# Kernel tuning notes

Hardware: AMD Instinct MI355X
Metric: run time of the kernel (lower is better)

The kernel has to match this reference:

```python
import jax, jax.numpy as jnp
import numpy as np

K = 5      # kernel_size
STRIDE = 1
EPS = 1e-7


def _extract_patches(x, k, s):
    # x: [B,H,W,C] -> [B,Ho,Wo,k,k,C], same (kh,kw,c) layout as tf.extract_image_patches VALID
    B, H, W, C = x.shape
    Ho = (H - k) // s + 1
    Wo = (W - k) // s + 1
    r = (jnp.arange(Ho) * s)[:, None] + jnp.arange(k)   # [Ho,k]
    c = (jnp.arange(Wo) * s)[:, None] + jnp.arange(k)   # [Wo,k]
    return x[:, r[:, None, :, None], c[None, :, None, :], :]


def _rotate(pflat, angle, k):
    # Replicates tf.contrib.image.transform with angles_to_projective_transforms,
    # including the (1+1e-7) normalization of the 3x3 matrix in the original code.
    # pflat: [N, k*k, C], angle: [N]; bilinear sampling, fill value 0 outside.
    N = pflat.shape[0]
    f32 = pflat.dtype
    co, si = jnp.cos(angle), jnp.sin(angle)
    km1 = jnp.asarray(k - 1, f32)
    xoff = (km1 - (co * km1 - si * km1)) * 0.5
    yoff = (km1 - (si * km1 + co * km1)) * 0.5
    scale = 1.0 / (1.0 + EPS)  # transforms /= transforms[:, 8:9] + 1e-7
    gy, gx = jnp.meshgrid(jnp.arange(k, dtype=f32), jnp.arange(k, dtype=f32), indexing='ij')
    sx = (co[:, None, None] * gx - si[:, None, None] * gy + xoff[:, None, None]) * scale
    sy = (si[:, None, None] * gx + co[:, None, None] * gy + yoff[:, None, None]) * scale
    sx = sx.reshape(N, k * k)
    sy = sy.reshape(N, k * k)
    x0 = jnp.floor(sx)
    y0 = jnp.floor(sy)
    wx = (sx - x0)[..., None]
    wy = (sy - y0)[..., None]
    x0i = x0.astype(jnp.int32)
    y0i = y0.astype(jnp.int32)

    def samp(yi, xi):
        valid = (xi >= 0) & (xi < k) & (yi >= 0) & (yi < k)
        idx = jnp.clip(yi, 0, k - 1) * k + jnp.clip(xi, 0, k - 1)   # [N,k*k]
        v = jnp.take_along_axis(pflat, idx[..., None], axis=1)      # [N,k*k,C]
        return jnp.where(valid[..., None], v, jnp.zeros((), f32))

    v00 = samp(y0i, x0i)
    v01 = samp(y0i, x0i + 1)
    v10 = samp(y0i + 1, x0i)
    v11 = samp(y0i + 1, x0i + 1)
    top = v00 * (1 - wx) + v01 * wx
    bot = v10 * (1 - wx) + v11 * wx
    return top * (1 - wy) + bot * wy   # [N,k*k,C]


def _forward(input_tensor, W, b):
    k, s = K, STRIDE
    B, H, Wd, C = input_tensor.shape
    patches = _extract_patches(input_tensor, k, s)      # [B,Ho,Wo,k,k,C]
    Ho, Wo = patches.shape[1], patches.shape[2]
    inten = patches.sum(-1)                             # [B,Ho,Wo,k,k] channel-sum intensity
    ridx = jnp.arange(k, dtype=patches.dtype)
    tot = inten.sum((-2, -1)) + EPS
    cr = (inten * ridx[:, None]).sum((-2, -1)) / tot    # centroid row
    cc = (inten * ridx[None, :]).sum((-2, -1)) / tot    # centroid col
    m = (k - 1) / 2.0                                   # meanCenter (same for row/col)
    angle = jnp.arctan2(cr - m, cc - m + EPS)           # [B,Ho,Wo]
    pflat = patches.reshape(B * Ho * Wo, k * k, C)
    rot = _rotate(pflat, angle.reshape(-1), k)          # [N,k*k,C]
    rot = rot.reshape(B, Ho * Wo, k * k * C)
    wflat = W.reshape(W.shape[0], -1)                   # [F, k*k*C]
    out = jnp.einsum('bpd,fd->bpf', rot, wflat)         # elementwise-mult-sum 'conv'
    return out.reshape(B, Ho, Wo, -1) + b


def setup_inputs():
    key = jax.random.key(0)
    k1, k2 = jax.random.split(key, 2)
    B, H, Wd, C, F = 4, 128, 128, 16, 32
    input_tensor = jax.random.uniform(k1, (B, H, Wd, C), dtype=jnp.float32)
    lim = float(np.sqrt(6.0 / (K * K * C + F)))  # glorot_uniform
    W = jax.random.uniform(k2, (F, K, K, C), minval=-lim, maxval=lim, dtype=jnp.float32)
    b = jnp.zeros((F,), jnp.float32)
    return {"input_tensor": input_tensor, "W": W, "b": b}


def reference(input_tensor, W, b):
    return _forward(input_tensor, W, b)
```

## Files before the change

kernel.cpp:

```cpp
#include <hip/hip_runtime.h>


#define KS     5
#define TILE   8
#define NPIX   64
#define TW     (TILE + KS - 1)
#define CPAD   20
#define C_IN   16
#define F_OUT  32
#define H_IN   128
#define W_IN   128
#define HO     124
#define WO     124
#define NBATCH 4
#define EPSF   1e-7f
#define BLOCK  256
#define NCHUNK 7
#define AROW   72
#define KW     400

typedef __attribute__((ext_vector_type(8))) short  short8;
typedef __attribute__((ext_vector_type(4))) float  floatx4;

static __device__ __forceinline__ short f2bf(float f) {
    union { float f; unsigned u; } v; v.f = f;
    unsigned r = v.u + 0x7fffu + ((v.u >> 16) & 1u);
    return (short)(r >> 16);
}

__global__ __launch_bounds__(BLOCK) void rotconv_kernel(
    const float* __restrict__ in, const float* __restrict__ Wg,
    const float* __restrict__ bg, float* __restrict__ out)
{
    __shared__ float s_in[TW * TW * CPAD];
    __shared__ float s_int[TW * (TW + 1)];
    __shared__ short sA[NPIX * AROW];

    const int tid  = threadIdx.x;
    const int bx = blockIdx.x, by = blockIdx.y, bimg = blockIdx.z;
    const int ox = bx * TILE, oy = by * TILE;

    const float* inb = in + (size_t)bimg * (H_IN * W_IN * C_IN);
    for (int i = tid; i < TW * TW * (C_IN / 4); i += BLOCK) {
        int cv = i & 3;
        int pp = i >> 2;
        int x = pp % TW, y = pp / TW;
        int gy = oy + y, gx = ox + x;
        float4 v = make_float4(0.f, 0.f, 0.f, 0.f);
        if (gy < H_IN && gx < W_IN)
            v = *(const float4*)(inb + ((size_t)(gy * W_IN + gx) * C_IN) + 4 * cv);
        *(float4*)(&s_in[pp * CPAD + 4 * cv]) = v;
    }
    __syncthreads();

    for (int pp = tid; pp < TW * TW; pp += BLOCK) {
        const float* sp = &s_in[pp * CPAD];
        float s = 0.f;
        #pragma unroll
        for (int c = 0; c < C_IN; ++c) s += sp[c];
        s_int[(pp / TW) * (TW + 1) + (pp % TW)] = s;
    }
    __syncthreads();

    const int p    = tid & 63;
    const int wv   = tid >> 6;
    const int lx   = p & 7, ly = p >> 3;
    const int col  = p & 15;
    const int quad = p >> 4;

    float tot = EPSF, cr = 0.f, cc = 0.f;
    #pragma unroll
    for (int dy = 0; dy < KS; ++dy)
        #pragma unroll
        for (int dx = 0; dx < KS; ++dx) {
            float v = s_int[(ly + dy) * (TW + 1) + (lx + dx)];
            tot += v; cr += v * (float)dy; cc += v * (float)dx;
        }
    cr /= tot; cc /= tot;
    float ang = atan2f(cr - 2.0f, cc - 2.0f + EPSF);
    float si, co;
    sincosf(ang, &si, &co);
    const float scl = 1.0f / (1.0f + EPSF);
    float xoff = (4.0f - (co * 4.0f - si * 4.0f)) * 0.5f;
    float yoff = (4.0f - (si * 4.0f + co * 4.0f)) * 0.5f;

    const int nt  = wv >> 1;
    const int mt0 = (wv & 1) * 2;

    floatx4 acc0, acc1;
    {
        float bv = bg[nt * 16 + col];
        acc0 = (floatx4){bv, bv, bv, bv};
        acc1 = acc0;
    }

    for (int ch = 0; ch < NCHUNK; ++ch) {
        int t = 4 * ch + wv;
        short8 alo = {0,0,0,0,0,0,0,0}, ahi = {0,0,0,0,0,0,0,0};
        if (t < KS * KS) {
            int ky = t / KS, kx = t - KS * ky;
            float sx = (co * (float)kx - si * (float)ky + xoff) * scl;
            float sy = (si * (float)kx + co * (float)ky + yoff) * scl;
            float fx0 = floorf(sx), fy0 = floorf(sy);
            float wx = sx - fx0, wy = sy - fy0;
            int x0 = (int)fx0, y0 = (int)fy0;
            int x1 = x0 + 1, y1 = y0 + 1;
            float vx0 = (x0 >= 0 && x0 < KS) ? 1.f : 0.f;
            float vx1 = (x1 >= 0 && x1 < KS) ? 1.f : 0.f;
            float vy0 = (y0 >= 0 && y0 < KS) ? 1.f : 0.f;
            float vy1 = (y1 >= 0 && y1 < KS) ? 1.f : 0.f;
            float w00 = (1.f - wx) * (1.f - wy) * vx0 * vy0;
            float w01 = wx * (1.f - wy) * vx1 * vy0;
            float w10 = (1.f - wx) * wy * vx0 * vy1;
            float w11 = wx * wy * vx1 * vy1;
            int cx0 = min(max(x0, 0), KS - 1), cx1 = min(max(x1, 0), KS - 1);
            int cy0 = min(max(y0, 0), KS - 1), cy1 = min(max(y1, 0), KS - 1);
            const float* p00 = &s_in[((ly + cy0) * TW + (lx + cx0)) * CPAD];
            const float* p01 = &s_in[((ly + cy0) * TW + (lx + cx1)) * CPAD];
            const float* p10 = &s_in[((ly + cy1) * TW + (lx + cx0)) * CPAD];
            const float* p11 = &s_in[((ly + cy1) * TW + (lx + cx1)) * CPAD];
            float r[16];
            #pragma unroll
            for (int cv = 0; cv < 4; ++cv) {
                float4 a = *(const float4*)(p00 + 4 * cv);
                float4 b = *(const float4*)(p01 + 4 * cv);
                float4 c = *(const float4*)(p10 + 4 * cv);
                float4 d = *(const float4*)(p11 + 4 * cv);
                r[4*cv+0] = w00 * a.x + w01 * b.x + w10 * c.x + w11 * d.x;
                r[4*cv+1] = w00 * a.y + w01 * b.y + w10 * c.y + w11 * d.y;
                r[4*cv+2] = w00 * a.z + w01 * b.z + w10 * c.z + w11 * d.z;
                r[4*cv+3] = w00 * a.w + w01 * b.w + w10 * c.w + w11 * d.w;
            }
            alo = (short8){f2bf(r[0]), f2bf(r[1]), f2bf(r[2]), f2bf(r[3]),
                           f2bf(r[4]), f2bf(r[5]), f2bf(r[6]), f2bf(r[7])};
            ahi = (short8){f2bf(r[8]),  f2bf(r[9]),  f2bf(r[10]), f2bf(r[11]),
                           f2bf(r[12]), f2bf(r[13]), f2bf(r[14]), f2bf(r[15])};
        }
        __syncthreads();
        *(short8*)(&sA[p * AROW + wv * 16])     = alo;
        *(short8*)(&sA[p * AROW + wv * 16 + 8]) = ahi;
        __syncthreads();

        int nk = (ch == NCHUNK - 1) ? 1 : 2;
        for (int kk = 0; kk < nk; ++kk) {
            int kg = ch * 64 + kk * 32 + quad * 8;
            short8 bf = {0,0,0,0,0,0,0,0};
            if (kg + 8 <= KW) {
                const float* wp = Wg + (size_t)(nt * 16 + col) * KW + kg;
                float4 a = *(const float4*)(wp);
                float4 b = *(const float4*)(wp + 4);
                bf = (short8){f2bf(a.x), f2bf(a.y), f2bf(a.z), f2bf(a.w),
                              f2bf(b.x), f2bf(b.y), f2bf(b.z), f2bf(b.w)};
            }
            short8 a0 = *(const short8*)(&sA[(16 * mt0 + col) * AROW + kk * 32 + quad * 8]);
            short8 a1 = *(const short8*)(&sA[(16 * mt0 + 16 + col) * AROW + kk * 32 + quad * 8]);
            acc0 = __builtin_amdgcn_mfma_f32_16x16x32_bf16(a0, bf, acc0, 0, 0, 0);
            acc1 = __builtin_amdgcn_mfma_f32_16x16x32_bf16(a1, bf, acc1, 0, 0, 0);
        }
    }

    #pragma unroll
    for (int r = 0; r < 4; ++r) {
        int pix0 = 16 * mt0 + quad * 4 + r;
        int ho = oy + (pix0 >> 3), wo = ox + (pix0 & 7);
        if (ho < HO && wo < WO)
            out[(((size_t)bimg * HO + ho) * WO + wo) * F_OUT + nt * 16 + col] = acc0[r];
        int pix1 = pix0 + 16;
        ho = oy + (pix1 >> 3); wo = ox + (pix1 & 7);
        if (ho < HO && wo < WO)
            out[(((size_t)bimg * HO + ho) * WO + wo) * F_OUT + nt * 16 + col] = acc1[r];
    }
}

extern "C" void kernel_launch(void* const* d_in, const int* in_sizes, int n_in,
                              void* d_out, int out_size, void* d_ws, size_t ws_size,
                              hipStream_t stream) {
    const float* in = (const float*)d_in[0];
    const float* Wg = (const float*)d_in[1];
    const float* bg = (const float*)d_in[2];
    float* out      = (float*)d_out;
    dim3 grid((WO + TILE - 1) / TILE, (HO + TILE - 1) / TILE, NBATCH);
    rotconv_kernel<<<grid, dim3(BLOCK), 0, stream>>>(in, Wg, bg, out);
}
```

Before: 76.15 us.

## Preload bf16 weight fragments into registers and double-buffer the A tile

Weight fragments for all K steps are loaded and converted to bf16 once at kernel start and kept in registers, rather than reloaded from global memory every chunk. The shared A tile is double-buffered, which removes one of the two barriers per chunk. The chunk loop is fully unrolled and launch bounds request 4 blocks per SM. The 13 short8 fragments add register pressure that could cut occupancy or cause spills.

```diff
diff --git a/kernel.cpp b/kernel.cpp
--- a/kernel.cpp
+++ b/kernel.cpp
@@ -16,6 +16,7 @@
 #define EPSF   1e-7f
 #define BLOCK  256
 #define NCHUNK 7
+#define NKSTEP 13
 #define AROW   72
 #define KW     400
 
@@ -28,17 +29,42 @@
     return (short)(r >> 16);
 }
 
-__global__ __launch_bounds__(BLOCK) void rotconv_kernel(
+__global__ __launch_bounds__(BLOCK, 4) void rotconv_kernel(
     const float* __restrict__ in, const float* __restrict__ Wg,
     const float* __restrict__ bg, float* __restrict__ out)
 {
     __shared__ float s_in[TW * TW * CPAD];
     __shared__ float s_int[TW * (TW + 1)];
-    __shared__ short sA[NPIX * AROW];
+    __shared__ short sA[2][NPIX * AROW];
 
     const int tid  = threadIdx.x;
     const int bx = blockIdx.x, by = blockIdx.y, bimg = blockIdx.z;
     const int ox = bx * TILE, oy = by * TILE;
+
+    const int p    = tid & 63;
+    const int wv   = tid >> 6;
+    const int lx   = p & 7, ly = p >> 3;
+    const int col  = p & 15;
+    const int quad = p >> 4;
+    const int nt   = wv >> 1;
+    const int mt0  = (wv & 1) * 2;
+
+    short8 wfrag[NKSTEP];
+    {
+        const float* wrow = Wg + (size_t)(nt * 16 + col) * KW;
+        #pragma unroll
+        for (int s = 0; s < NKSTEP; ++s) {
+            int kg = s * 32 + quad * 8;
+            short8 bf = {0,0,0,0,0,0,0,0};
+            if (kg + 8 <= KW) {
+                float4 a = *(const float4*)(wrow + kg);
+                float4 b = *(const float4*)(wrow + kg + 4);
+                bf = (short8){f2bf(a.x), f2bf(a.y), f2bf(a.z), f2bf(a.w),
+                              f2bf(b.x), f2bf(b.y), f2bf(b.z), f2bf(b.w)};
+            }
+            wfrag[s] = bf;
+        }
+    }
 
     const float* inb = in + (size_t)bimg * (H_IN * W_IN * C_IN);
     for (int i = tid; i < TW * TW * (C_IN / 4); i += BLOCK) {
@@ -62,12 +88,6 @@
     }
     __syncthreads();
 
-    const int p    = tid & 63;
-    const int wv   = tid >> 6;
-    const int lx   = p & 7, ly = p >> 3;
-    const int col  = p & 15;
-    const int quad = p >> 4;
-
     float tot = EPSF, cr = 0.f, cc = 0.f;
     #pragma unroll
     for (int dy = 0; dy < KS; ++dy)
@@ -84,9 +104,6 @@
     float xoff = (4.0f - (co * 4.0f - si * 4.0f)) * 0.5f;
     float yoff = (4.0f - (si * 4.0f + co * 4.0f)) * 0.5f;
 
-    const int nt  = wv >> 1;
-    const int mt0 = (wv & 1) * 2;
-
     floatx4 acc0, acc1;
     {
         float bv = bg[nt * 16 + col];
@@ -94,6 +111,7 @@
         acc1 = acc0;
     }
 
+    #pragma unroll
     for (int ch = 0; ch < NCHUNK; ++ch) {
         int t = 4 * ch + wv;
         short8 alo = {0,0,0,0,0,0,0,0}, ahi = {0,0,0,0,0,0,0,0};
@@ -136,26 +154,20 @@
             ahi = (short8){f2bf(r[8]),  f2bf(r[9]),  f2bf(r[10]), f2bf(r[11]),
                            f2bf(r[12]), f2bf(r[13]), f2bf(r[14]), f2bf(r[15])};
         }
-        __syncthreads();
-        *(short8*)(&sA[p * AROW + wv * 16])     = alo;
-        *(short8*)(&sA[p * AROW + wv * 16 + 8]) = ahi;
+        short* buf = &sA[ch & 1][0];
+        *(short8*)(&buf[p * AROW + wv * 16])     = alo;
+        *(short8*)(&buf[p * AROW + wv * 16 + 8]) = ahi;
         __syncthreads();
 
-        int nk = (ch == NCHUNK - 1) ? 1 : 2;
-        for (int kk = 0; kk < nk; ++kk) {
-            int kg = ch * 64 + kk * 32 + quad * 8;
-            short8 bf = {0,0,0,0,0,0,0,0};
-            if (kg + 8 <= KW) {
-                const float* wp = Wg + (size_t)(nt * 16 + col) * KW + kg;
-                float4 a = *(const float4*)(wp);
-                float4 b = *(const float4*)(wp + 4);
-                bf = (short8){f2bf(a.x), f2bf(a.y), f2bf(a.z), f2bf(a.w),
-                              f2bf(b.x), f2bf(b.y), f2bf(b.z), f2bf(b.w)};
+        #pragma unroll
+        for (int kk = 0; kk < 2; ++kk) {
+            int s = ch * 2 + kk;
+            if (s < NKSTEP) {
+                short8 a0 = *(const short8*)(&buf[(16 * mt0 + col) * AROW + kk * 32 + quad * 8]);
+                short8 a1 = *(const short8*)(&buf[(16 * mt0 + 16 + col) * AROW + kk * 32 + quad * 8]);
+                acc0 = __builtin_amdgcn_mfma_f32_16x16x32_bf16(a0, wfrag[s], acc0, 0, 0, 0);
+                acc1 = __builtin_amdgcn_mfma_f32_16x16x32_bf16(a1, wfrag[s], acc1, 0, 0, 0);
             }
-            short8 a0 = *(const short8*)(&sA[(16 * mt0 + col) * AROW + kk * 32 + quad * 8]);
-            short8 a1 = *(const short8*)(&sA[(16 * mt0 + 16 + col) * AROW + kk * 32 + quad * 8]);
-            acc0 = __builtin_amdgcn_mfma_f32_16x16x32_bf16(a0, bf, acc0, 0, 0, 0);
-            acc1 = __builtin_amdgcn_mfma_f32_16x16x32_bf16(a1, bf, acc1, 0, 0, 0);
         }
     }
 
```

After: 90.36 us. 1.19x slower.

## Split-K across waves with 32x32 MFMA and shared bf16 weights

Applied to the files above, without the earlier changes.

Each wave now keeps the samples it computes for its own filter taps in registers and runs 32x32x16 bf16 MFMAs over all 64 pixels and 32 filters. This removes the per-chunk LDS staging of the A operand and the two barriers per chunk. The bf16-converted weights are preloaded once per block into shared memory, and the four partial accumulators are reduced through LDS at the end, with wave 0 adding the bias and writing the output. The trade-offs are larger accumulators (32 VGPRs per wave), a final LDS reduction, a cross-lane shuffle to assemble the A fragments, and a launch-bounds occupancy hint.

```diff
diff --git a/kernel.cpp b/kernel.cpp
--- a/kernel.cpp
+++ b/kernel.cpp
@@ -3,7 +3,6 @@
 
 #define KS     5
 #define TILE   8
-#define NPIX   64
 #define TW     (TILE + KS - 1)
 #define CPAD   20
 #define C_IN   16
@@ -15,30 +14,48 @@
 #define NBATCH 4
 #define EPSF   1e-7f
 #define BLOCK  256
-#define NCHUNK 7
-#define AROW   72
+#define NTAP   25
 #define KW     400
 
-typedef __attribute__((ext_vector_type(8))) short  short8;
-typedef __attribute__((ext_vector_type(4))) float  floatx4;
+typedef __attribute__((ext_vector_type(8)))  short short8;
+typedef __attribute__((ext_vector_type(16))) float floatx16;
 
-static __device__ __forceinline__ short f2bf(float f) {
+static __device__ __forceinline__ unsigned f2bfu(float f) {
     union { float f; unsigned u; } v; v.f = f;
     unsigned r = v.u + 0x7fffu + ((v.u >> 16) & 1u);
-    return (short)(r >> 16);
+    return r >> 16;
+}
+static __device__ __forceinline__ unsigned pack2(float a, float b) {
+    return f2bfu(a) | (f2bfu(b) << 16);
 }
 
-__global__ __launch_bounds__(BLOCK) void rotconv_kernel(
+__global__ __launch_bounds__(BLOCK, 4) void rotconv_kernel(
     const float* __restrict__ in, const float* __restrict__ Wg,
     const float* __restrict__ bg, float* __restrict__ out)
 {
     __shared__ float s_in[TW * TW * CPAD];
     __shared__ float s_int[TW * (TW + 1)];
-    __shared__ short sA[NPIX * AROW];
+    __shared__ union {
+        short w[NTAP * 64 * 8];
+        float red[3 * 2048];
+    } uW;
 
     const int tid  = threadIdx.x;
     const int bx = blockIdx.x, by = blockIdx.y, bimg = blockIdx.z;
     const int ox = bx * TILE, oy = by * TILE;
+    const int p  = tid & 63;
+    const int wv = __builtin_amdgcn_readfirstlane(tid >> 6);
+    const int lx = p & 7, ly = p >> 3;
+
+    for (int i = tid; i < NTAP * 64; i += BLOCK) {
+        int t = i >> 6, l = i & 63;
+        const float* wp = Wg + (size_t)(l & 31) * KW + t * 16 + (l >> 5) * 8;
+        float4 a = *(const float4*)(wp);
+        float4 b = *(const float4*)(wp + 4);
+        unsigned* d = (unsigned*)&uW.w[i * 8];
+        d[0] = pack2(a.x, a.y); d[1] = pack2(a.z, a.w);
+        d[2] = pack2(b.x, b.y); d[3] = pack2(b.z, b.w);
+    }
 
     const float* inb = in + (size_t)bimg * (H_IN * W_IN * C_IN);
     for (int i = tid; i < TW * TW * (C_IN / 4); i += BLOCK) {
@@ -62,12 +79,6 @@
     }
     __syncthreads();
 
-    const int p    = tid & 63;
-    const int wv   = tid >> 6;
-    const int lx   = p & 7, ly = p >> 3;
-    const int col  = p & 15;
-    const int quad = p >> 4;
-
     float tot = EPSF, cr = 0.f, cc = 0.f;
     #pragma unroll
     for (int dy = 0; dy < KS; ++dy)
@@ -84,20 +95,11 @@
     float xoff = (4.0f - (co * 4.0f - si * 4.0f)) * 0.5f;
     float yoff = (4.0f - (si * 4.0f + co * 4.0f)) * 0.5f;
 
-    const int nt  = wv >> 1;
-    const int mt0 = (wv & 1) * 2;
+    floatx16 acc0 = {0}, acc1 = {0};
 
-    floatx4 acc0, acc1;
-    {
-        float bv = bg[nt * 16 + col];
-        acc0 = (floatx4){bv, bv, bv, bv};
-        acc1 = acc0;
-    }
-
-    for (int ch = 0; ch < NCHUNK; ++ch) {
-        int t = 4 * ch + wv;
-        short8 alo = {0,0,0,0,0,0,0,0}, ahi = {0,0,0,0,0,0,0,0};
-        if (t < KS * KS) {
+    for (int i = 0; i < 7; ++i) {
+        int t = wv + 4 * i;
+        if (t < NTAP) {
             int ky = t / KS, kx = t - KS * ky;
             float sx = (co * (float)kx - si * (float)ky + xoff) * scl;
             float sy = (si * (float)kx + co * (float)ky + yoff) * scl;
@@ -131,44 +133,54 @@
                 r[4*cv+2] = w00 * a.z + w01 * b.z + w10 * c.z + w11 * d.z;
                 r[4*cv+3] = w00 * a.w + w01 * b.w + w10 * c.w + w11 * d.w;
             }
-            alo = (short8){f2bf(r[0]), f2bf(r[1]), f2bf(r[2]), f2bf(r[3]),
-                           f2bf(r[4]), f2bf(r[5]), f2bf(r[6]), f2bf(r[7])};
-            ahi = (short8){f2bf(r[8]),  f2bf(r[9]),  f2bf(r[10]), f2bf(r[11]),
-                           f2bf(r[12]), f2bf(r[13]), f2bf(r[14]), f2bf(r[15])};
-        }
-        __syncthreads();
-        *(short8*)(&sA[p * AROW + wv * 16])     = alo;
-        *(short8*)(&sA[p * AROW + wv * 16 + 8]) = ahi;
-        __syncthreads();
-
-        int nk = (ch == NCHUNK - 1) ? 1 : 2;
-        for (int kk = 0; kk < nk; ++kk) {
-            int kg = ch * 64 + kk * 32 + quad * 8;
-            short8 bf = {0,0,0,0,0,0,0,0};
-            if (kg + 8 <= KW) {
-                const float* wp = Wg + (size_t)(nt * 16 + col) * KW + kg;
-                float4 a = *(const float4*)(wp);
-                float4 b = *(const float4*)(wp + 4);
-                bf = (short8){f2bf(a.x), f2bf(a.y), f2bf(a.z), f2bf(a.w),
-                              f2bf(b.x), f2bf(b.y), f2bf(b.z), f2bf(b.w)};
+            unsigned lo[4], hi[4];
+            #pragma unroll
+            for (int d = 0; d < 4; ++d) {
+                lo[d] = pack2(r[2*d],     r[2*d + 1]);
+                hi[d] = pack2(r[8 + 2*d], r[9 + 2*d]);
             }
-            short8 a0 = *(const short8*)(&sA[(16 * mt0 + col) * AROW + kk * 32 + quad * 8]);
-            short8 a1 = *(const short8*)(&sA[(16 * mt0 + 16 + col) * AROW + kk * 32 + quad * 8]);
-            acc0 = __builtin_amdgcn_mfma_f32_16x16x32_bf16(a0, bf, acc0, 0, 0, 0);
-            acc1 = __builtin_amdgcn_mfma_f32_16x16x32_bf16(a1, bf, acc1, 0, 0, 0);
+            union { unsigned u[4]; short8 v; } a0, a1;
+            #pragma unroll
+            for (int d = 0; d < 4; ++d) {
+                unsigned snd = (p < 32) ? hi[d] : lo[d];
+                unsigned rcv = (unsigned)__shfl((int)snd, p ^ 32, 64);
+                a0.u[d] = (p < 32) ? lo[d] : rcv;
+                a1.u[d] = (p < 32) ? rcv : hi[d];
+            }
+            short8 bf = *(const short8*)(&uW.w[(t * 64 + p) * 8]);
+            acc0 = __builtin_amdgcn_mfma_f32_32x32x16_bf16(a0.v, bf, acc0, 0, 0, 0);
+            acc1 = __builtin_amdgcn_mfma_f32_32x32x16_bf16(a1.v, bf, acc1, 0, 0, 0);
         }
     }
 
-    #pragma unroll
-    for (int r = 0; r < 4; ++r) {
-        int pix0 = 16 * mt0 + quad * 4 + r;
-        int ho = oy + (pix0 >> 3), wo = ox + (pix0 & 7);
-        if (ho < HO && wo < WO)
-            out[(((size_t)bimg * HO + ho) * WO + wo) * F_OUT + nt * 16 + col] = acc0[r];
-        int pix1 = pix0 + 16;
-        ho = oy + (pix1 >> 3); wo = ox + (pix1 & 7);
-        if (ho < HO && wo < WO)
-            out[(((size_t)bimg * HO + ho) * WO + wo) * F_OUT + nt * 16 + col] = acc1[r];
+    __syncthreads();
+    if (wv > 0) {
+        float* red = &uW.red[(wv - 1) * 2048];
+        #pragma unroll
+        for (int r = 0; r < 16; ++r) {
+            red[r * 64 + p]         = acc0[r];
+            red[(16 + r) * 64 + p]  = acc1[r];
+        }
+    }
+    __syncthreads();
+
+    if (wv == 0) {
+        float bias = bg[p & 31];
+        #pragma unroll
+        for (int T = 0; T < 2; ++T) {
+            #pragma unroll
+            for (int r = 0; r < 16; ++r) {
+                int s = T * 16 + r;
+                float v = (T == 0 ? acc0[r] : acc1[r])
+                        + uW.red[s * 64 + p]
+                        + uW.red[2048 + s * 64 + p]
+                        + uW.red[4096 + s * 64 + p] + bias;
+                int px = T * 32 + (r & 3) + 8 * (r >> 2) + 4 * (p >> 5);
+                int ho = oy + (px >> 3), wo = ox + (px & 7);
+                if (ho < HO && wo < WO)
+                    out[(((size_t)bimg * HO + ho) * WO + wo) * F_OUT + (p & 31)] = v;
+            }
+        }
     }
 }
 
```

After: 80.88 us. 1.06x slower.
